# Performance work log

Hardware: AMD Instinct MI355X
Metric: run time of the kernel (lower is better)

## Reference

```python
import jax, jax.numpy as jnp
import numpy as np

B, T, C, H = 4, 2048, 1024, 16
HD = C // H  # head dim = 64


def setup_inputs() -> dict:
    key = jax.random.key(0)
    k1, k2, k3, k4, k5 = jax.random.split(key, 5)
    s_in = 1.0 / np.sqrt(C)
    return {
        "x": jax.random.normal(k1, (B, T, C), dtype=jnp.float32),
        "W_attn": jax.random.uniform(k2, (C, 3 * C), dtype=jnp.float32, minval=-s_in, maxval=s_in),
        "b_attn": jax.random.uniform(k3, (3 * C,), dtype=jnp.float32, minval=-s_in, maxval=s_in),
        "W_proj": jax.random.uniform(k4, (C, C), dtype=jnp.float32, minval=-s_in, maxval=s_in),
        "b_proj": jax.random.uniform(k5, (C,), dtype=jnp.float32, minval=-s_in, maxval=s_in),
    }


def reference(x, W_attn, b_attn, W_proj, b_proj):
    Bx, Tx, Cx = x.shape
    qkv = x @ W_attn + b_attn                      # [B,T,3C]
    q, k, v = jnp.split(qkv, 3, axis=2)
    # [B,T,C] -> [B,H,T,HD]
    def heads(t):
        return t.reshape(Bx, Tx, H, HD).transpose(0, 2, 1, 3)
    q, k, v = heads(q), heads(k), heads(v)
    scale = 1.0 / np.sqrt(HD).astype(np.float32)
    att = jnp.einsum('bhqd,bhkd->bhqk', q, k) * scale
    causal = jnp.tril(jnp.ones((Tx, Tx), dtype=bool))
    att = jnp.where(causal[None, None], att, -jnp.inf)
    att = jax.nn.softmax(att, axis=-1)
    y = jnp.einsum('bhqk,bhkd->bhqd', att, v)      # [B,H,T,HD]
    y = y.transpose(0, 2, 1, 3).reshape(Bx, Tx, Cx)
    return y @ W_proj + b_proj
```

## Files before the change

### kernel.cpp

```cpp
#include <hip/hip_runtime.h>
#include <math.h>

#define Bn 4
#define Tn 2048
#define Cn 1024
#define Hn 16
#define HDn 64
#define Mn (Bn * Tn)

typedef unsigned short u16;
typedef unsigned int u32;
typedef __attribute__((ext_vector_type(8))) short bf16x8;
typedef __attribute__((ext_vector_type(8))) unsigned short us8;
typedef __attribute__((ext_vector_type(4))) float f32x4;
typedef __attribute__((ext_vector_type(16))) float f32x16;
typedef __attribute__((ext_vector_type(4))) unsigned int u32x4;

__device__ __forceinline__ float b2f(u16 u) {
    return __uint_as_float(((u32)u) << 16);
}
__device__ __forceinline__ u16 f2b(float f) {
    u32 u = __float_as_uint(f);
    return (u16)((u + 0x7FFFu + ((u >> 16) & 1u)) >> 16);
}
__device__ __forceinline__ u32 cvtpk(float a, float b) {
    u32 d;
    asm("v_cvt_pk_bf16_f32 %0, %1, %2" : "=v"(d) : "v"(a), "v"(b));
    return d;
}
__device__ __forceinline__ void pswap(u32& a, u32& b) {
    asm("v_permlane32_swap_b32 %0, %1" : "+v"(a), "+v"(b));
}

__device__ __forceinline__ int xcd_work(int bid, int nwg) {
    return (bid & 7) * (nwg >> 3) + (bid >> 3);
}

#define GLL(srcp, dstp)                                                     \
    __builtin_amdgcn_global_load_lds(                                       \
        (const __attribute__((address_space(1))) u32*)(srcp),               \
        (__attribute__((address_space(3))) u32*)(dstp), 16, 0, 0)

__global__ __launch_bounds__(256) void cvt_f32_bf16_kernel(
    const float4* __restrict__ in, ushort4* __restrict__ out, int n4)
{
    for (int i = blockIdx.x * 256 + threadIdx.x; i < n4; i += gridDim.x * 256) {
        float4 v = in[i];
        ushort4 o;
        o.x = f2b(v.x); o.y = f2b(v.y); o.z = f2b(v.z); o.w = f2b(v.w);
        out[i] = o;
    }
}

__global__ __launch_bounds__(256) void transpose_cvt_kernel(
    const float* __restrict__ in, u16* __restrict__ out, int R, int Cc)
{
    __shared__ u16 t[32][33];
    const int c0 = blockIdx.x * 32, r0 = blockIdx.y * 32;
    const int tx = threadIdx.x & 31, ty = threadIdx.x >> 5;
    #pragma unroll
    for (int i = 0; i < 32; i += 8)
        t[ty + i][tx] = f2b(in[(size_t)(r0 + ty + i) * Cc + c0 + tx]);
    __syncthreads();
    #pragma unroll
    for (int i = 0; i < 32; i += 8)
        out[(size_t)(c0 + ty + i) * R + r0 + tx] = t[tx][ty + i];
}

template <bool OUT_BF16, bool QKV_MODE>
__global__ __launch_bounds__(256) void gemm_bf16_kernel(
    const u16* __restrict__ A, const u16* __restrict__ BT,
    const float* __restrict__ bias,
    u16* __restrict__ outb, float* __restrict__ outf, u16* __restrict__ vTout,
    int N, int K, int nx)
{
    __shared__ u16 Al[2][128 * 32];
    __shared__ u16 Bl[2][128 * 32];

    const int tid = threadIdx.x;
    const int workid = xcd_work(blockIdx.x, gridDim.x);
    const int brow = (workid / nx) * 128;
    const int bcol = (workid % nx) * 128;
    const int w  = tid >> 6;
    const int wr = w >> 1, wc = w & 1;
    const int l  = tid & 63;
    const int lr = l & 15;
    const int lk = (l >> 4) << 3;

    const int r0s = tid >> 2,            c0s = (tid & 3) << 3;
    const int r1s = (256 + tid) >> 2,    c1s = c0s;
    const int d0s = (tid & 192) * 8;
    const int d1s = (256 + (tid & 192)) * 8;

    f32x4 acc[4][4];
    #pragma unroll
    for (int m = 0; m < 4; ++m)
        #pragma unroll
        for (int n = 0; n < 4; ++n) acc[m][n] = (f32x4){0.f, 0.f, 0.f, 0.f};

    GLL(&A [(size_t)(brow + r0s) * K + c0s], &Al[0][d0s]);
    GLL(&BT[(size_t)(bcol + r0s) * K + c0s], &Bl[0][d0s]);
    GLL(&A [(size_t)(brow + r1s) * K + c1s], &Al[0][d1s]);
    GLL(&BT[(size_t)(bcol + r1s) * K + c1s], &Bl[0][d1s]);
    __syncthreads();

    int cur = 0;
    for (int k0 = 0; k0 < K; k0 += 32) {
        if (k0 + 32 < K) {
            const int kn = k0 + 32;
            GLL(&A [(size_t)(brow + r0s) * K + kn + c0s], &Al[cur ^ 1][d0s]);
            GLL(&BT[(size_t)(bcol + r0s) * K + kn + c0s], &Bl[cur ^ 1][d0s]);
            GLL(&A [(size_t)(brow + r1s) * K + kn + c1s], &Al[cur ^ 1][d1s]);
            GLL(&BT[(size_t)(bcol + r1s) * K + kn + c1s], &Bl[cur ^ 1][d1s]);
        }

        bf16x8 a[4], b[4];
        #pragma unroll
        for (int m = 0; m < 4; ++m)
            a[m] = *(const bf16x8*)&Al[cur][(wr * 64 + m * 16 + lr) * 32 + lk];
        #pragma unroll
        for (int n = 0; n < 4; ++n)
            b[n] = *(const bf16x8*)&Bl[cur][(wc * 64 + n * 16 + lr) * 32 + lk];

        __builtin_amdgcn_s_setprio(1);
        #pragma unroll
        for (int m = 0; m < 4; ++m)
            #pragma unroll
            for (int n = 0; n < 4; ++n)
                acc[m][n] = __builtin_amdgcn_mfma_f32_16x16x32_bf16(
                    a[m], b[n], acc[m][n], 0, 0, 0);
        __builtin_amdgcn_s_setprio(0);

        __syncthreads();
        cur ^= 1;
    }

    const int orow0 = brow + wr * 64 + ((l >> 4) << 2);
    const int ocol0 = bcol + wc * 64 + lr;
    if (QKV_MODE && bcol >= 2048) {
        #pragma unroll
        for (int n = 0; n < 4; ++n) {
            const int c = ocol0 + n * 16 - 2048;
            const float bv = bias[ocol0 + n * 16];
            #pragma unroll
            for (int m = 0; m < 4; ++m) {
                const int row0 = orow0 + m * 16;
                const int bb = row0 >> 11, t0 = row0 & 2047;
                ushort4 pk;
                pk.x = f2b(acc[m][n][0] + bv);
                pk.y = f2b(acc[m][n][1] + bv);
                pk.z = f2b(acc[m][n][2] + bv);
                pk.w = f2b(acc[m][n][3] + bv);
                *(ushort4*)&vTout[((size_t)bb * Cn + c) * Tn + t0] = pk;
            }
        }
    } else {
        #pragma unroll
        for (int n = 0; n < 4; ++n) {
            const int col = ocol0 + n * 16;
            const float bv = bias[col];
            #pragma unroll
            for (int m = 0; m < 4; ++m) {
                #pragma unroll
                for (int r = 0; r < 4; ++r) {
                    const int row = orow0 + m * 16 + r;
                    const float v = acc[m][n][r] + bv;
                    if (OUT_BF16) outb[(size_t)row * N + col] = f2b(v);
                    else          outf[(size_t)row * N + col] = v;
                }
            }
        }
    }
}

__global__ __launch_bounds__(256, 2) void attn_mfma6_kernel(
    const u16* __restrict__ qkvb, const u16* __restrict__ vT,
    u16* __restrict__ yb)
{
    __shared__ u16 Kb[2][64 * 64];
    __shared__ u16 Vb[2][64 * 64];

    const int tid = threadIdx.x;
    const int w   = tid >> 6;
    const int l   = tid & 63;
    const int q31 = l & 31;
    const int hi  = l >> 5;
    const int work = xcd_work(blockIdx.x, 512);
    const int pr  = work & 7;
    const int bh  = work >> 3;
    const int b   = bh >> 4, h = bh & 15;

    const float S2 = 0.18033688f;

    const u16* Kg = qkvb + (size_t)(b * Tn) * (3 * Cn) + Cn + h * HDn;
    const u16* Vg = vT + (size_t)bh * HDn * Tn;

    const int srow = l >> 3;
    const int schk = ((l & 7) ^ srow) << 3;
    const int rloc = w * 16;
    const int rsw8 = q31 & 7;

    #pragma unroll 1
    for (int half = 0; half < 2; ++half) {
        const int qt = half ? (15 - pr) : pr;
        const int ktmax = 2 * qt + 2;
        const int qrow0 = qt * 128 + w * 32;
        const int qglob = qrow0 + q31;

        const u16* Qp = qkvb + (size_t)(b * Tn + qglob) * (3 * Cn)
                        + h * HDn + hi * 8;
        bf16x8 qf[4];
        #pragma unroll
        for (int c = 0; c < 4; ++c) qf[c] = *(const bf16x8*)(Qp + c * 16);

        f32x16 O0, O1;
        #pragma unroll
        for (int r = 0; r < 16; ++r) { O0[r] = 0.f; O1[r] = 0.f; }
        float m = -INFINITY, ls = 0.f;

        #pragma unroll
        for (int jc = 0; jc < 2; ++jc) {
            const int rr = rloc + jc * 8;
            GLL(Kg + (size_t)(rr + srow) * (3 * Cn) + schk, &Kb[0][rr * 64]);
            GLL(Vg + (size_t)(rr + srow) * Tn + schk,       &Vb[0][rr * 64]);
        }
        __syncthreads();

        int cur = 0;
        for (int kt = 0; kt < ktmax; ++kt) {
            if (kt + 1 < ktmax) {
                #pragma unroll
                for (int jc = 0; jc < 2; ++jc) {
                    const int rr = rloc + jc * 8;
                    GLL(Kg + (size_t)((kt + 1) * 64 + rr + srow) * (3 * Cn) + schk,
                        &Kb[cur ^ 1][rr * 64]);
                    GLL(Vg + (size_t)(rr + srow) * Tn + (kt + 1) * 64 + schk,
                        &Vb[cur ^ 1][rr * 64]);
                }
            }
            const u16* Kc = Kb[cur];
            const u16* Vc = Vb[cur];

            if (kt * 64 <= qrow0 + 31) {
                f32x16 S0, S1;
                #pragma unroll
                for (int r = 0; r < 16; ++r) { S0[r] = 0.f; S1[r] = 0.f; }
                __builtin_amdgcn_s_setprio(1);
                #pragma unroll
                for (int c = 0; c < 4; ++c) {
                    const int co = ((2 * c + hi) ^ rsw8) << 3;
                    const bf16x8 k0 = *(const bf16x8*)&Kc[q31 * 64 + co];
                    const bf16x8 k1 = *(const bf16x8*)&Kc[(32 + q31) * 64 + co];
                    S0 = __builtin_amdgcn_mfma_f32_32x32x16_bf16(k0, qf[c], S0, 0, 0, 0);
                    S1 = __builtin_amdgcn_mfma_f32_32x32x16_bf16(k1, qf[c], S1, 0, 0, 0);
                }
                __builtin_amdgcn_s_setprio(0);

                if (kt * 64 + 63 > qrow0) {
                    #pragma unroll
                    for (int r = 0; r < 16; ++r) {
                        const int kl = kt * 64 + (r & 3) + 8 * (r >> 2) + 4 * hi;
                        if (kl > qglob)      S0[r] = -INFINITY;
                        if (kl + 32 > qglob) S1[r] = -INFINITY;
                    }
                }

                float mt = S0[0];
                #pragma unroll
                for (int r = 1; r < 16; ++r) mt = fmaxf(mt, S0[r]);
                #pragma unroll
                for (int r = 0; r < 16; ++r) mt = fmaxf(mt, S1[r]);
                mt = fmaxf(mt, __shfl_xor(mt, 32));

                float lscale = 1.f;
                if (__any(mt > m + 64.f)) {
                    const float mn = fmaxf(m, mt);
                    const float alpha = exp2f((m - mn) * S2);
                    m = mn; lscale = alpha;
                    #pragma unroll
                    for (int r = 0; r < 16; ++r) {
                        const int qloc = (r & 3) + 8 * (r >> 2) + 4 * hi;
                        const float ar = __shfl(alpha, qloc);
                        O0[r] *= ar; O1[r] *= ar;
                    }
                }

                float lt = 0.f;
                u32 w0[8], w1[8];
                #pragma unroll
                for (int i = 0; i < 8; ++i) {
                    const float p0 = exp2f((S0[2 * i]     - m) * S2);
                    const float p1 = exp2f((S0[2 * i + 1] - m) * S2);
                    const float p2 = exp2f((S1[2 * i]     - m) * S2);
                    const float p3 = exp2f((S1[2 * i + 1] - m) * S2);
                    lt += (p0 + p1) + (p2 + p3);
                    w0[i] = cvtpk(p0, p1);
                    w1[i] = cvtpk(p2, p3);
                }
                lt += __shfl_xor(lt, 32);
                ls = ls * lscale + lt;

                __builtin_amdgcn_s_setprio(1);
                #pragma unroll
                for (int t2 = 0; t2 < 2; ++t2) {
                    #pragma unroll
                    for (int c1 = 0; c1 < 2; ++c1) {
                        u32 a0 = t2 ? w1[4 * c1 + 0] : w0[4 * c1 + 0];
                        u32 b0 = t2 ? w1[4 * c1 + 2] : w0[4 * c1 + 2];
                        u32 a1 = t2 ? w1[4 * c1 + 1] : w0[4 * c1 + 1];
                        u32 b1 = t2 ? w1[4 * c1 + 3] : w0[4 * c1 + 3];
                        pswap(a0, b0);
                        pswap(a1, b1);
                        u32x4 fr; fr.x = a0; fr.y = a1; fr.z = b0; fr.w = b1;
                        const bf16x8 pf = __builtin_bit_cast(bf16x8, fr);
                        const int c = t2 * 2 + c1;
                        const int co = ((2 * c + hi) ^ rsw8) << 3;
                        const bf16x8 v0 = *(const bf16x8*)&Vc[q31 * 64 + co];
                        const bf16x8 v1 = *(const bf16x8*)&Vc[(32 + q31) * 64 + co];
                        O0 = __builtin_amdgcn_mfma_f32_32x32x16_bf16(pf, v0, O0, 0, 0, 0);
                        O1 = __builtin_amdgcn_mfma_f32_32x32x16_bf16(pf, v1, O1, 0, 0, 0);
                    }
                }
                __builtin_amdgcn_s_setprio(0);
            }

            __syncthreads();
            cur ^= 1;
        }

        #pragma unroll
        for (int r = 0; r < 16; ++r) {
            const int qloc = (r & 3) + 8 * (r >> 2) + 4 * hi;
            const float inv = __builtin_amdgcn_rcpf(__shfl(ls, qloc));
            u16* yp = yb + (size_t)(b * Tn + qrow0 + qloc) * Cn + h * HDn + q31;
            yp[0]  = f2b(O0[r] * inv);
            yp[32] = f2b(O1[r] * inv);
        }
    }
}

extern "C" void kernel_launch(void* const* d_in, const int* in_sizes, int n_in,
                              void* d_out, int out_size, void* d_ws, size_t ws_size,
                              hipStream_t stream)
{
    const float* x      = (const float*)d_in[0];
    const float* W_attn = (const float*)d_in[1];
    const float* b_attn = (const float*)d_in[2];
    const float* W_proj = (const float*)d_in[3];
    const float* b_proj = (const float*)d_in[4];
    float* out = (float*)d_out;

    u16* xb   = (u16*)d_ws;
    u16* WaT  = xb   + (size_t)Mn * Cn;
    u16* WpT  = WaT  + (size_t)3 * Cn * Cn;
    u16* qkvb = WpT  + (size_t)Cn * Cn;
    u16* yb   = qkvb + (size_t)Mn * 3 * Cn;
    u16* vT   = yb   + (size_t)Mn * Cn;

    cvt_f32_bf16_kernel<<<2048, 256, 0, stream>>>(
        (const float4*)x, (ushort4*)xb, Mn * Cn / 4);

    transpose_cvt_kernel<<<dim3(3 * Cn / 32, Cn / 32), 256, 0, stream>>>(
        W_attn, WaT, Cn, 3 * Cn);
    transpose_cvt_kernel<<<dim3(Cn / 32, Cn / 32), 256, 0, stream>>>(
        W_proj, WpT, Cn, Cn);

    gemm_bf16_kernel<true, true><<<24 * 64, 256, 0, stream>>>(
        xb, WaT, b_attn, qkvb, nullptr, vT, 3 * Cn, Cn, 24);

    attn_mfma6_kernel<<<512, 256, 0, stream>>>(qkvb, vT, yb);

    gemm_bf16_kernel<false, false><<<8 * 64, 256, 0, stream>>>(
        yb, WpT, b_proj, nullptr, out, nullptr, Cn, Cn, 8);
}
```

Measured before the change: 200.7 us.

## Triple-buffer GEMM and attention LDS loads with vmcnt waits and one barrier

Converts both the bf16 GEMM and the flash-attention kernel from double-buffered to triple-buffered LDS staging. Loads are issued two tiles ahead, and the full __syncthreads pair is replaced by a partial s_waitcnt vmcnt plus a single s_barrier per iteration. The goal is to keep more global-to-LDS traffic in flight and cut barrier stalls. This raises LDS usage per block, which could lower occupancy. Correctness also depends on the hand-written vmcnt counts matching the number of outstanding loads.

```diff
diff --git a/kernel.cpp b/kernel.cpp
--- a/kernel.cpp
+++ b/kernel.cpp
@@ -40,6 +40,9 @@
     __builtin_amdgcn_global_load_lds(                                       \
         (const __attribute__((address_space(1))) u32*)(srcp),               \
         (__attribute__((address_space(3))) u32*)(dstp), 16, 0, 0)
+
+#define WAITCNT4() asm volatile("s_waitcnt vmcnt(4)" ::: "memory")
+#define WAITCNT0() asm volatile("s_waitcnt vmcnt(0)" ::: "memory")
 
 __global__ __launch_bounds__(256) void cvt_f32_bf16_kernel(
     const float4* __restrict__ in, ushort4* __restrict__ out, int n4)
@@ -74,8 +77,8 @@
     u16* __restrict__ outb, float* __restrict__ outf, u16* __restrict__ vTout,
     int N, int K, int nx)
 {
-    __shared__ u16 Al[2][128 * 32];
-    __shared__ u16 Bl[2][128 * 32];
+    __shared__ u16 Al[3][128 * 32];
+    __shared__ u16 Bl[3][128 * 32];
 
     const int tid = threadIdx.x;
     const int workid = xcd_work(blockIdx.x, gridDim.x);
@@ -88,7 +91,7 @@
     const int lk = (l >> 4) << 3;
 
     const int r0s = tid >> 2,            c0s = (tid & 3) << 3;
-    const int r1s = (256 + tid) >> 2,    c1s = c0s;
+    const int r1s = (256 + tid) >> 2;
     const int d0s = (tid & 192) * 8;
     const int d1s = (256 + (tid & 192)) * 8;
 
@@ -98,20 +101,27 @@
         #pragma unroll
         for (int n = 0; n < 4; ++n) acc[m][n] = (f32x4){0.f, 0.f, 0.f, 0.f};
 
-    GLL(&A [(size_t)(brow + r0s) * K + c0s], &Al[0][d0s]);
-    GLL(&BT[(size_t)(bcol + r0s) * K + c0s], &Bl[0][d0s]);
-    GLL(&A [(size_t)(brow + r1s) * K + c1s], &Al[0][d1s]);
-    GLL(&BT[(size_t)(bcol + r1s) * K + c1s], &Bl[0][d1s]);
-    __syncthreads();
+    #define STAGE_G(k0, bufi)                                                \
+        do {                                                                 \
+            GLL(&A [(size_t)(brow + r0s) * K + (k0) + c0s], &Al[bufi][d0s]); \
+            GLL(&BT[(size_t)(bcol + r0s) * K + (k0) + c0s], &Bl[bufi][d0s]); \
+            GLL(&A [(size_t)(brow + r1s) * K + (k0) + c0s], &Al[bufi][d1s]); \
+            GLL(&BT[(size_t)(bcol + r1s) * K + (k0) + c0s], &Bl[bufi][d1s]); \
+        } while (0)
+
+    const int T = K >> 5;
+    STAGE_G(0, 0);
+    STAGE_G(32, 1);
 
     int cur = 0;
-    for (int k0 = 0; k0 < K; k0 += 32) {
-        if (k0 + 32 < K) {
-            const int kn = k0 + 32;
-            GLL(&A [(size_t)(brow + r0s) * K + kn + c0s], &Al[cur ^ 1][d0s]);
-            GLL(&BT[(size_t)(bcol + r0s) * K + kn + c0s], &Bl[cur ^ 1][d0s]);
-            GLL(&A [(size_t)(brow + r1s) * K + kn + c1s], &Al[cur ^ 1][d1s]);
-            GLL(&BT[(size_t)(bcol + r1s) * K + kn + c1s], &Bl[cur ^ 1][d1s]);
+    for (int t = 0; t < T; ++t) {
+        if (t < T - 1) WAITCNT4();
+        else           WAITCNT0();
+        __builtin_amdgcn_s_barrier();
+
+        if (t + 2 < T) {
+            const int nb = cur + 2 >= 3 ? cur - 1 : cur + 2;
+            STAGE_G((t + 2) << 5, nb);
         }
 
         bf16x8 a[4], b[4];
@@ -131,9 +141,9 @@
                     a[m], b[n], acc[m][n], 0, 0, 0);
         __builtin_amdgcn_s_setprio(0);
 
-        __syncthreads();
-        cur ^= 1;
+        cur = cur == 2 ? 0 : cur + 1;
     }
+    #undef STAGE_G
 
     const int orow0 = brow + wr * 64 + ((l >> 4) << 2);
     const int ocol0 = bcol + wc * 64 + lr;
@@ -173,12 +183,12 @@
     }
 }
 
-__global__ __launch_bounds__(256, 2) void attn_mfma6_kernel(
+__global__ __launch_bounds__(256, 2) void attn_mfma7_kernel(
     const u16* __restrict__ qkvb, const u16* __restrict__ vT,
     u16* __restrict__ yb)
 {
-    __shared__ u16 Kb[2][64 * 64];
-    __shared__ u16 Vb[2][64 * 64];
+    __shared__ u16 Kb[3][64 * 64];
+    __shared__ u16 Vb[3][64 * 64];
 
     const int tid = threadIdx.x;
     const int w   = tid >> 6;
@@ -200,6 +210,18 @@
     const int rloc = w * 16;
     const int rsw8 = q31 & 7;
 
+    #define STAGE_A(kt, bufi)                                                  \
+        do {                                                                   \
+            _Pragma("unroll")                                                  \
+            for (int jc = 0; jc < 2; ++jc) {                                   \
+                const int rr = rloc + jc * 8;                                  \
+                GLL(Kg + (size_t)((kt) * 64 + rr + srow) * (3 * Cn) + schk,    \
+                    &Kb[bufi][rr * 64]);                                       \
+                GLL(Vg + (size_t)(rr + srow) * Tn + (kt) * 64 + schk,          \
+                    &Vb[bufi][rr * 64]);                                       \
+            }                                                                  \
+        } while (0)
+
     #pragma unroll 1
     for (int half = 0; half < 2; ++half) {
         const int qt = half ? (15 - pr) : pr;
@@ -218,25 +240,18 @@
         for (int r = 0; r < 16; ++r) { O0[r] = 0.f; O1[r] = 0.f; }
         float m = -INFINITY, ls = 0.f;
 
-        #pragma unroll
-        for (int jc = 0; jc < 2; ++jc) {
-            const int rr = rloc + jc * 8;
-            GLL(Kg + (size_t)(rr + srow) * (3 * Cn) + schk, &Kb[0][rr * 64]);
-            GLL(Vg + (size_t)(rr + srow) * Tn + schk,       &Vb[0][rr * 64]);
-        }
-        __syncthreads();
+        STAGE_A(0, 0);
+        STAGE_A(1, 1);
 
         int cur = 0;
         for (int kt = 0; kt < ktmax; ++kt) {
-            if (kt + 1 < ktmax) {
-                #pragma unroll
-                for (int jc = 0; jc < 2; ++jc) {
-                    const int rr = rloc + jc * 8;
-                    GLL(Kg + (size_t)((kt + 1) * 64 + rr + srow) * (3 * Cn) + schk,
-                        &Kb[cur ^ 1][rr * 64]);
-                    GLL(Vg + (size_t)(rr + srow) * Tn + (kt + 1) * 64 + schk,
-                        &Vb[cur ^ 1][rr * 64]);
-                }
+            if (kt < ktmax - 1) WAITCNT4();
+            else                WAITCNT0();
+            __builtin_amdgcn_s_barrier();
+
+            if (kt + 2 < ktmax) {
+                const int nb = cur + 2 >= 3 ? cur - 1 : cur + 2;
+                STAGE_A(kt + 2, nb);
             }
             const u16* Kc = Kb[cur];
             const u16* Vc = Vb[cur];
@@ -324,9 +339,10 @@
                 __builtin_amdgcn_s_setprio(0);
             }
 
-            __syncthreads();
-            cur ^= 1;
-        }
+            cur = cur == 2 ? 0 : cur + 1;
+        }
+
+        __builtin_amdgcn_s_barrier();
 
         #pragma unroll
         for (int r = 0; r < 16; ++r) {
@@ -337,6 +353,7 @@
             yp[32] = f2b(O1[r] * inv);
         }
     }
+    #undef STAGE_A
 }
 
 extern "C" void kernel_launch(void* const* d_in, const int* in_sizes, int n_in,
@@ -368,7 +385,7 @@
     gemm_bf16_kernel<true, true><<<24 * 64, 256, 0, stream>>>(
         xb, WaT, b_attn, qkvb, nullptr, vT, 3 * Cn, Cn, 24);
 
-    attn_mfma6_kernel<<<512, 256, 0, stream>>>(qkvb, vT, yb);
+    attn_mfma7_kernel<<<512, 256, 0, stream>>>(qkvb, vT, yb);
 
     gemm_bf16_kernel<false, false><<<8 * 64, 256, 0, stream>>>(
         yb, WpT, b_proj, nullptr, out, nullptr, Cn, Cn, 8);
```

Result: no change. 200.9 us (+0.1%).
